# Kernel optimization log

Hardware: AMD Instinct MI355X
Metric: run time of the kernel (lower is better)

Reference implementation:

```python
import jax, jax.numpy as jnp
import numpy as np

B, S, H = 2, 2048, 2048
NH, HD = 16, 128


def _rope_tables(seq_len, dim, base=10000.0):
    inv_freq = 1.0 / (base ** (np.arange(0, dim, 2, dtype=np.float32) / dim))
    t = np.arange(seq_len, dtype=np.float32)
    freqs = np.outer(t, inv_freq)                      # [S, dim/2]
    emb = np.concatenate([freqs, freqs], axis=-1)      # [S, dim] (HF convention)
    return jnp.asarray(np.cos(emb)), jnp.asarray(np.sin(emb))


def setup_inputs() -> dict:
    key = jax.random.key(0)
    k1, k2, k3, k4, k5 = jax.random.split(key, 5)
    hidden_states = jax.random.normal(k1, (B, S, H), dtype=jnp.float32)
    # additive causal mask, broadcast over heads: (B, 1, S, S)
    causal = jnp.tril(jnp.ones((S, S), dtype=bool))
    attention_mask = jnp.where(causal, 0.0, -1e9).astype(jnp.float32)
    attention_mask = jnp.broadcast_to(attention_mask[None, None], (B, 1, S, S))
    rope_cos, rope_sin = _rope_tables(S, HD)
    scale = 1.0 / np.sqrt(H)
    Wq = jax.random.normal(k2, (H, H), dtype=jnp.float32) * scale
    Wk = jax.random.normal(k3, (H, H), dtype=jnp.float32) * scale
    Wv = jax.random.normal(k4, (H, H), dtype=jnp.float32) * scale
    Wo = jax.random.normal(k5, (H, H), dtype=jnp.float32) * scale
    return dict(hidden_states=hidden_states, attention_mask=attention_mask,
                rope_cos=rope_cos, rope_sin=rope_sin, Wq=Wq, Wk=Wk, Wv=Wv, Wo=Wo)


def _rotate_half(x):
    half = x.shape[-1] // 2
    return jnp.concatenate([-x[..., half:], x[..., :half]], axis=-1)


def reference(hidden_states, attention_mask, rope_cos, rope_sin, Wq, Wk, Wv, Wo):
    bsz, q_len, _ = hidden_states.shape
    scaling = HD ** -0.5
    # projections (torch Linear: y = x @ W.T)
    q = (hidden_states @ Wq.T).reshape(bsz, q_len, NH, HD).transpose(0, 2, 1, 3)
    k = (hidden_states @ Wk.T).reshape(bsz, q_len, NH, HD).transpose(0, 2, 1, 3)
    v = (hidden_states @ Wv.T).reshape(bsz, q_len, NH, HD).transpose(0, 2, 1, 3)
    # RoPE (rotate_half convention)
    cos = rope_cos[None, None]  # [1,1,S,HD]
    sin = rope_sin[None, None]
    q = q * cos + _rotate_half(q) * sin
    k = k * cos + _rotate_half(k) * sin
    # attention
    scores = jnp.einsum('bhqd,bhkd->bhqk', q, k) * scaling + attention_mask
    attn = jax.nn.softmax(scores.astype(jnp.float32), axis=-1).astype(q.dtype)
    out = jnp.einsum('bhqk,bhkd->bhqd', attn, v)
    out = out.transpose(0, 2, 1, 3).reshape(bsz, q_len, NH * HD)
    return out @ Wo.T
```

## Files before the change

### kernel.cpp

```cpp
#include <hip/hip_runtime.h>
#include <hip/hip_bf16.h>

typedef __bf16 bf16;
typedef __attribute__((ext_vector_type(8))) __bf16 bf16x8;
typedef __attribute__((ext_vector_type(4))) __bf16 bf16x4;
typedef __attribute__((ext_vector_type(4))) float f32x4;

#define BB 2
#define SS 2048
#define HH 2048
#define NH 16
#define HD 128

#define GLOAD_LDS16(g, l)                                                  \
    __builtin_amdgcn_global_load_lds(                                      \
        (const __attribute__((address_space(1))) void*)(g),                \
        (__attribute__((address_space(3))) void*)(l), 16, 0, 0)

__global__ __launch_bounds__(256) void cast_all(const float* __restrict__ hs,
                                                const float* __restrict__ Wq,
                                                const float* __restrict__ Wk,
                                                const float* __restrict__ Wv,
                                                const float* __restrict__ Wo,
                                                bf16* __restrict__ Xb,
                                                bf16* __restrict__ Wqkv,
                                                bf16* __restrict__ Wob) {
    const int XE4 = (BB * SS * HH) / 4;
    const int WE4 = (HH * HH) / 4;
    int i = blockIdx.x * 256 + threadIdx.x;
    const float* src;
    bf16* dst;
    int off;
    if (i < XE4) { src = hs; dst = Xb; off = i; }
    else if (i < XE4 + WE4) { src = Wq; dst = Wqkv; off = i - XE4; }
    else if (i < XE4 + 2 * WE4) { src = Wk; dst = Wqkv + (size_t)HH * HH; off = i - XE4 - WE4; }
    else if (i < XE4 + 3 * WE4) { src = Wv; dst = Wqkv + 2 * (size_t)HH * HH; off = i - XE4 - 2 * WE4; }
    else { src = Wo; dst = Wob; off = i - XE4 - 3 * WE4; }
    f32x4 v = *reinterpret_cast<const f32x4*>(src + (size_t)off * 4);
    bf16x4 o;
    o[0] = (bf16)v[0]; o[1] = (bf16)v[1]; o[2] = (bf16)v[2]; o[3] = (bf16)v[3];
    *reinterpret_cast<bf16x4*>(dst + (size_t)off * 4) = o;
}

__global__ __launch_bounds__(512, 2) void gemm256_qkv(const bf16* __restrict__ A,
                                                      const bf16* __restrict__ B,
                                                      bf16* __restrict__ Cb,
                                                      int M, int N, int K) {
    __shared__ bf16 LA[2][256 * 64];
    __shared__ bf16 LB[2][192 * 64];
    const int tid = threadIdx.x, lane = tid & 63, wave = tid >> 6;
    const int l15 = lane & 15, lhi = lane >> 4;
    const int wr = wave >> 2, wc = wave & 3;
    const int cpx = gridDim.x >> 3;
    const int wg = (blockIdx.x & 7) * cpx + (blockIdx.x >> 3);
    const int m0 = (wg & 15) * 256, n0 = (wg >> 4) * 192;
    const int NK = K >> 6;
    const int xorR = (l15 & 7) << 4;

    auto stageA = [&](int buf, int t, int h) {
        const int k0 = t << 6;
#pragma unroll
        for (int j = 0; j < 2; ++j) {
            int Xw = (h * 128 + j * 64 + wave * 8) << 7;
            int X = Xw + lane * 16;
            int T = X ^ (((X >> 7) & 7) << 4);
            GLOAD_LDS16(&A[(size_t)(m0 + (T >> 7)) * K + k0 + ((T & 127) >> 1)],
                        (char*)LA[buf] + Xw);
        }
    };
    auto stageB = [&](int buf, int t, int s) {
        const int k0 = t << 6;
        int row_base = (wave >> 1) * 48 + s * 16 + (wave & 1) * 8;
        int Xw = row_base << 7;
        int X = Xw + lane * 16;
        int T = X ^ (((X >> 7) & 7) << 4);
        GLOAD_LDS16(&B[(size_t)(n0 + (T >> 7)) * K + k0 + ((T & 127) >> 1)],
                    (char*)LB[buf] + Xw);
    };

    f32x4 acc[8][3] = {};

    stageA(0, 0, 0); stageA(0, 0, 1);
    stageB(0, 0, 0); stageB(0, 0, 1); stageB(0, 0, 2);
    stageA(1, 1, 0); stageA(1, 1, 1);
    stageB(1, 1, 0); stageB(1, 1, 1);
    asm volatile("s_waitcnt vmcnt(6)" ::: "memory");
    __builtin_amdgcn_s_barrier();

    bf16x8 af[8][2], bv[2];

#pragma unroll 1
    for (int t = 0; t < NK; ++t) {
        const int buf = t & 1;
        char* lA = (char*)LA[buf];
        char* lB = (char*)LB[buf];

#pragma unroll
        for (int mf = 0; mf < 8; ++mf)
#pragma unroll
            for (int ks = 0; ks < 2; ++ks) {
                int T = ((wr * 128 + mf * 16 + l15) << 7) + ks * 64 + lhi * 16;
                af[mf][ks] = *reinterpret_cast<const bf16x8*>(lA + (T ^ xorR));
            }
#pragma unroll
        for (int ks = 0; ks < 2; ++ks) {
            int T = ((wc * 48 + l15) << 7) + ks * 64 + lhi * 16;
            bv[ks] = *reinterpret_cast<const bf16x8*>(lB + (T ^ xorR));
        }
        if (t + 1 < NK) stageB(buf ^ 1, t + 1, 2);
        __builtin_amdgcn_s_barrier();
        __builtin_amdgcn_s_setprio(1);
#pragma unroll
        for (int mf = 0; mf < 8; ++mf)
#pragma unroll
            for (int ks = 0; ks < 2; ++ks)
                acc[mf][0] = __builtin_amdgcn_mfma_f32_16x16x32_bf16(af[mf][ks], bv[ks], acc[mf][0], 0, 0, 0);
        __builtin_amdgcn_s_setprio(0);
        __builtin_amdgcn_s_barrier();

#pragma unroll
        for (int ks = 0; ks < 2; ++ks) {
            int T = ((wc * 48 + 16 + l15) << 7) + ks * 64 + lhi * 16;
            bv[ks] = *reinterpret_cast<const bf16x8*>(lB + (T ^ xorR));
        }
        if (t + 2 < NK) { stageB(buf, t + 2, 0); stageA(buf, t + 2, 0); }
        __builtin_amdgcn_s_barrier();
        __builtin_amdgcn_s_setprio(1);
#pragma unroll
        for (int mf = 0; mf < 8; ++mf)
#pragma unroll
            for (int ks = 0; ks < 2; ++ks)
                acc[mf][1] = __builtin_amdgcn_mfma_f32_16x16x32_bf16(af[mf][ks], bv[ks], acc[mf][1], 0, 0, 0);
        __builtin_amdgcn_s_setprio(0);
        __builtin_amdgcn_s_barrier();

#pragma unroll
        for (int ks = 0; ks < 2; ++ks) {
            int T = ((wc * 48 + 32 + l15) << 7) + ks * 64 + lhi * 16;
            bv[ks] = *reinterpret_cast<const bf16x8*>(lB + (T ^ xorR));
        }
        if (t + 2 < NK) { stageB(buf, t + 2, 1); stageA(buf, t + 2, 1); }
        __builtin_amdgcn_s_barrier();
        __builtin_amdgcn_s_setprio(1);
#pragma unroll
        for (int mf = 0; mf < 8; ++mf)
#pragma unroll
            for (int ks = 0; ks < 2; ++ks)
                acc[mf][2] = __builtin_amdgcn_mfma_f32_16x16x32_bf16(af[mf][ks], bv[ks], acc[mf][2], 0, 0, 0);
        __builtin_amdgcn_s_setprio(0);
        if (t + 2 < NK) {
            asm volatile("s_waitcnt vmcnt(6)" ::: "memory");
        } else if (t + 2 == NK) {
            asm volatile("s_waitcnt vmcnt(0)" ::: "memory");
        }
        __builtin_amdgcn_s_barrier();
    }

#pragma unroll
    for (int mf = 0; mf < 8; ++mf)
#pragma unroll
        for (int nsl = 0; nsl < 3; ++nsl)
#pragma unroll
            for (int r = 0; r < 4; ++r) {
                int gm = m0 + wr * 128 + mf * 16 + lhi * 4 + r;
                int gn = n0 + wc * 48 + nsl * 16 + l15;
                int proj = gn >> 11, n2 = gn & 2047;
                int b = gm >> 11, s = gm & (SS - 1);
                int h = n2 >> 7, d = n2 & (HD - 1);
                Cb[((size_t)proj << 23) + ((((size_t)(b * NH + h)) * SS + s) << 7) + d] =
                    (bf16)acc[mf][nsl][r];
            }
}

__global__ __launch_bounds__(512, 2) void gemm_op(const bf16* __restrict__ A,
                                                  const bf16* __restrict__ B,
                                                  float* __restrict__ Cf,
                                                  int M, int N, int K) {
    __shared__ bf16 LA[2][256 * 64];
    __shared__ bf16 LB[2][128 * 64];
    const int tid = threadIdx.x, lane = tid & 63, wave = tid >> 6;
    const int l15 = lane & 15, lhi = lane >> 4;
    const int wr = wave >> 2, wc = wave & 3;
    const int cpx = gridDim.x >> 3;
    const int wg = (blockIdx.x & 7) * cpx + (blockIdx.x >> 3);
    const int m0 = (wg & 15) * 256, n0 = (wg >> 4) * 128;
    const int NK = K >> 6;
    const int xorR = (l15 & 7) << 4;

    auto stageA = [&](int buf, int t, int h) {
        const int k0 = t << 6;
#pragma unroll
        for (int j = 0; j < 2; ++j) {
            int Xw = (h * 128 + j * 64 + wave * 8) << 7;
            int X = Xw + lane * 16;
            int T = X ^ (((X >> 7) & 7) << 4);
            GLOAD_LDS16(&A[(size_t)(m0 + (T >> 7)) * K + k0 + ((T & 127) >> 1)],
                        (char*)LA[buf] + Xw);
        }
    };
    auto stageB = [&](int buf, int t, int s) {
        const int k0 = t << 6;
        int row_base = (wave >> 1) * 32 + s * 16 + (wave & 1) * 8;
        int Xw = row_base << 7;
        int X = Xw + lane * 16;
        int T = X ^ (((X >> 7) & 7) << 4);
        GLOAD_LDS16(&B[(size_t)(n0 + (T >> 7)) * K + k0 + ((T & 127) >> 1)],
                    (char*)LB[buf] + Xw);
    };

    f32x4 acc[8][2] = {};

    stageA(0, 0, 0); stageA(0, 0, 1); stageB(0, 0, 0); stageB(0, 0, 1);
    stageA(1, 1, 0); stageA(1, 1, 1); stageB(1, 1, 0);
    asm volatile("s_waitcnt vmcnt(5)" ::: "memory");
    __builtin_amdgcn_s_barrier();

    bf16x8 af[8][2], bv[2];

#pragma unroll 1
    for (int t = 0; t < NK; ++t) {
        const int buf = t & 1;
        char* lA = (char*)LA[buf];
        char* lB = (char*)LB[buf];

#pragma unroll
        for (int mf = 0; mf < 8; ++mf)
#pragma unroll
            for (int ks = 0; ks < 2; ++ks) {
                int T = ((wr * 128 + mf * 16 + l15) << 7) + ks * 64 + lhi * 16;
                af[mf][ks] = *reinterpret_cast<const bf16x8*>(lA + (T ^ xorR));
            }
#pragma unroll
        for (int ks = 0; ks < 2; ++ks) {
            int T = ((wc * 32 + l15) << 7) + ks * 64 + lhi * 16;
            bv[ks] = *reinterpret_cast<const bf16x8*>(lB + (T ^ xorR));
        }
        if (t + 1 < NK) stageB(buf ^ 1, t + 1, 1);
        __builtin_amdgcn_s_barrier();
        __builtin_amdgcn_s_setprio(1);
#pragma unroll
        for (int mf = 0; mf < 8; ++mf)
#pragma unroll
            for (int ks = 0; ks < 2; ++ks)
                acc[mf][0] = __builtin_amdgcn_mfma_f32_16x16x32_bf16(af[mf][ks], bv[ks], acc[mf][0], 0, 0, 0);
        __builtin_amdgcn_s_setprio(0);
        __builtin_amdgcn_s_barrier();

#pragma unroll
        for (int ks = 0; ks < 2; ++ks) {
            int T = ((wc * 32 + 16 + l15) << 7) + ks * 64 + lhi * 16;
            bv[ks] = *reinterpret_cast<const bf16x8*>(lB + (T ^ xorR));
        }
        if (t + 2 < NK) { stageB(buf, t + 2, 0); stageA(buf, t + 2, 0); stageA(buf, t + 2, 1); }
        __builtin_amdgcn_s_barrier();
        __builtin_amdgcn_s_setprio(1);
#pragma unroll
        for (int mf = 0; mf < 8; ++mf)
#pragma unroll
            for (int ks = 0; ks < 2; ++ks)
                acc[mf][1] = __builtin_amdgcn_mfma_f32_16x16x32_bf16(af[mf][ks], bv[ks], acc[mf][1], 0, 0, 0);
        __builtin_amdgcn_s_setprio(0);
        if (t + 2 < NK) {
            asm volatile("s_waitcnt vmcnt(5)" ::: "memory");
        } else {
            asm volatile("s_waitcnt vmcnt(0)" ::: "memory");
        }
        __builtin_amdgcn_s_barrier();
    }

#pragma unroll
    for (int mf = 0; mf < 8; ++mf)
#pragma unroll
        for (int nsl = 0; nsl < 2; ++nsl)
#pragma unroll
            for (int r = 0; r < 4; ++r) {
                int gm = m0 + wr * 128 + mf * 16 + lhi * 4 + r;
                int gn = n0 + wc * 32 + nsl * 16 + l15;
                Cf[(size_t)gm * N + gn] = acc[mf][nsl][r];
            }
}

__global__ __launch_bounds__(256) void rope_tv(bf16* __restrict__ Qh,
                                               bf16* __restrict__ Kh,
                                               const float* __restrict__ cosT,
                                               const float* __restrict__ sinT,
                                               const bf16* __restrict__ Vh,
                                               bf16* __restrict__ Vt) {
    __shared__ bf16 T[64 * 64];
    const int tid = threadIdx.x;
    if (blockIdx.x < 2048) {
        int idx = blockIdx.x * 256 + tid;
        int g = idx & 7;
        int s = (idx >> 3) & (SS - 1);
        int head = idx >> 14;
        int d0 = g * 8;
        size_t base = ((size_t)head * SS + s) * HD;
        f32x4 ca = *reinterpret_cast<const f32x4*>(&cosT[s * HD + d0]);
        f32x4 cb = *reinterpret_cast<const f32x4*>(&cosT[s * HD + d0 + 4]);
        f32x4 sa = *reinterpret_cast<const f32x4*>(&sinT[s * HD + d0]);
        f32x4 sb = *reinterpret_cast<const f32x4*>(&sinT[s * HD + d0 + 4]);
        bf16x8 ql = *reinterpret_cast<const bf16x8*>(&Qh[base + d0]);
        bf16x8 qh = *reinterpret_cast<const bf16x8*>(&Qh[base + 64 + d0]);
        bf16x8 kl = *reinterpret_cast<const bf16x8*>(&Kh[base + d0]);
        bf16x8 kh = *reinterpret_cast<const bf16x8*>(&Kh[base + 64 + d0]);
        bf16x8 qlo, qhi, klo, khi;
#pragma unroll
        for (int j = 0; j < 8; ++j) {
            float c = (j < 4) ? ca[j] : cb[j - 4];
            float sn = (j < 4) ? sa[j] : sb[j - 4];
            float q0 = (float)ql[j], q1 = (float)qh[j];
            float k0 = (float)kl[j], k1 = (float)kh[j];
            qlo[j] = (bf16)(q0 * c - q1 * sn);
            qhi[j] = (bf16)(q1 * c + q0 * sn);
            klo[j] = (bf16)(k0 * c - k1 * sn);
            khi[j] = (bf16)(k1 * c + k0 * sn);
        }
        *reinterpret_cast<bf16x8*>(&Qh[base + d0]) = qlo;
        *reinterpret_cast<bf16x8*>(&Qh[base + 64 + d0]) = qhi;
        *reinterpret_cast<bf16x8*>(&Kh[base + d0]) = klo;
        *reinterpret_cast<bf16x8*>(&Kh[base + 64 + d0]) = khi;
    } else {
        const int b2 = blockIdx.x - 2048;
        const int s0 = (b2 & 31) * 64;
        const int d0 = ((b2 >> 5) & 1) * 64;
        const int head = b2 >> 6;
        const bf16* src = Vh + ((size_t)head * SS) * HD;
        bf16* dst = Vt + ((size_t)head * HD) * SS;

#pragma unroll
        for (int i = 0; i < 2; ++i) {
            int id = tid + i * 256;
            int r = id >> 3, c16 = id & 7;
            bf16x8 v = *reinterpret_cast<const bf16x8*>(&src[(size_t)(s0 + r) * HD + d0 + c16 * 8]);
            int sw = c16 ^ ((r ^ (r >> 3)) & 7);
            *reinterpret_cast<bf16x8*>((char*)T + r * 128 + sw * 16) = v;
        }
        __syncthreads();
#pragma unroll
        for (int i = 0; i < 2; ++i) {
            int id = tid + i * 256;
            int dr = id >> 3, sc8 = (id & 7) * 8;
            bf16x8 o;
#pragma unroll
            for (int j = 0; j < 8; ++j) {
                int r = sc8 + j;
                int sw = (dr >> 3) ^ ((r ^ (r >> 3)) & 7);
                o[j] = *reinterpret_cast<const bf16*>((char*)T + r * 128 + sw * 16 + (dr & 7) * 2);
            }
            *reinterpret_cast<bf16x8*>(&dst[(size_t)(d0 + dr) * SS + s0 + sc8]) = o;
        }
    }
}

__global__ __launch_bounds__(256) void attn_kernel(const bf16* __restrict__ Q,
                                                   const bf16* __restrict__ K,
                                                   const bf16* __restrict__ Vt,
                                                   bf16* __restrict__ Ob) {
    __shared__ bf16 Ks[2][64 * 128];
    __shared__ bf16 Vs[2][128 * 64];
    __shared__ bf16 Ps[4][32 * 72];

    const int tid = threadIdx.x, lane = tid & 63, wave = tid >> 6;
    const int l15 = lane & 15, lhi = lane >> 4;
    const int bid = blockIdx.x;
    const int orig = (bid & 7) * 32 + (bid >> 3);
    const int head = orig >> 3;
    const int pi = orig & 7;
    const int b = head >> 4, h = head & (NH - 1);
    const size_t hb = (size_t)head * SS * HD;
    const bf16* Vth = Vt + (size_t)head * HD * SS;
    const float cexp = 0.08838834764831845f * 1.4426950408889634f;
    const float THR = 62.0f;

    auto stageKV = [&](int buf, int kv0) {
#pragma unroll
        for (int j = 0; j < 4; ++j) {
            int Xw = (j * 4 + wave) << 10;
            int X = Xw + lane * 16;
            int T = X ^ (((X >> 8) & 7) << 4);
            GLOAD_LDS16(&K[hb + (size_t)(kv0 + (T >> 8)) * HD + ((T & 255) >> 1)],
                        (char*)Ks[buf] + Xw);
        }
#pragma unroll
        for (int j = 0; j < 4; ++j) {
            int Xw = (j * 4 + wave) << 10;
            int X = Xw + lane * 16;
            int T = X ^ (((X >> 7) & 7) << 4);
            GLOAD_LDS16(&Vth[(size_t)(T >> 7) * SS + kv0 + ((T & 127) >> 1)],
                        (char*)Vs[buf] + Xw);
        }
    };

#pragma unroll 1
    for (int part = 0; part < 2; ++part) {
        const int t = part ? (15 - pi) : pi;
        const int q0 = t * 128;
        const int qw0 = q0 + wave * 32;
        const int nkv = 2 * t + 2;

        bf16x8 qf[2][4];
#pragma unroll
        for (int mf = 0; mf < 2; ++mf)
#pragma unroll
            for (int ks = 0; ks < 4; ++ks)
                qf[mf][ks] = *reinterpret_cast<const bf16x8*>(
                    &Q[hb + (size_t)(qw0 + mf * 16 + l15) * HD + ks * 32 + 8 * lhi]);

        f32x4 oacc[2][8] = {};
        float Mr[2][4], Lp[2][4];
#pragma unroll
        for (int mf = 0; mf < 2; ++mf)
#pragma unroll
            for (int r = 0; r < 4; ++r) { Mr[mf][r] = -INFINITY; Lp[mf][r] = 0.f; }

        stageKV(0, 0);
        asm volatile("s_waitcnt vmcnt(0)" ::: "memory");
        __builtin_amdgcn_s_barrier();

        for (int it = 0; it < nkv; ++it) {
            const int cur = it & 1;
            if (it + 1 < nkv) stageKV(cur ^ 1, (it + 1) * 64);

            f32x4 sf[2][4] = {};
#pragma unroll
            for (int ks = 0; ks < 4; ++ks) {
#pragma unroll
                for (int ne = 0; ne < 4; ++ne) {
                    int row = ne * 16 + l15;
                    bf16x8 kf = *reinterpret_cast<const bf16x8*>(
                        (const char*)Ks[cur] + ((row * 256 + (ks * 4 + lhi) * 16) ^ ((row & 7) << 4)));
#pragma unroll
                    for (int mf = 0; mf < 2; ++mf)
                        sf[mf][ne] = __builtin_amdgcn_mfma_f32_16x16x32_bf16(qf[mf][ks], kf, sf[mf][ne], 0, 0, 0);
                }
            }

            if (it >= nkv - 2) {
#pragma unroll
                for (int mf = 0; mf < 2; ++mf)
#pragma unroll
                    for (int ne = 0; ne < 4; ++ne)
#pragma unroll
                        for (int r = 0; r < 4; ++r) {
                            int gq = qw0 + mf * 16 + lhi * 4 + r;
                            int gk = it * 64 + ne * 16 + l15;
                            if (gk > gq) sf[mf][ne][r] = -INFINITY;
                        }
            }

            float lm[2][4];
            bool need = false;
#pragma unroll
            for (int mf = 0; mf < 2; ++mf)
#pragma unroll
                for (int r = 0; r < 4; ++r) {
                    lm[mf][r] = fmaxf(fmaxf(sf[mf][0][r], sf[mf][1][r]),
                                      fmaxf(sf[mf][2][r], sf[mf][3][r]));
                    need = need || (lm[mf][r] > Mr[mf][r] + THR);
                }
            if (__any(need)) {
                float rmax[2][4];
#pragma unroll
                for (int mf = 0; mf < 2; ++mf)
#pragma unroll
                    for (int r = 0; r < 4; ++r) rmax[mf][r] = lm[mf][r];
#pragma unroll
                for (int m = 1; m < 16; m <<= 1)
#pragma unroll
                    for (int mf = 0; mf < 2; ++mf)
#pragma unroll
                        for (int r = 0; r < 4; ++r)
                            rmax[mf][r] = fmaxf(rmax[mf][r], __shfl_xor(rmax[mf][r], m));
#pragma unroll
                for (int mf = 0; mf < 2; ++mf)
#pragma unroll
                    for (int r = 0; r < 4; ++r) {
                        float nM = fmaxf(Mr[mf][r], rmax[mf][r]);
                        float scf = __builtin_amdgcn_exp2f((Mr[mf][r] - nM) * cexp);
                        Mr[mf][r] = nM;
                        Lp[mf][r] *= scf;
#pragma unroll
                        for (int nf = 0; nf < 8; ++nf) oacc[mf][nf][r] *= scf;
                    }
            }
#pragma unroll
            for (int mf = 0; mf < 2; ++mf)
#pragma unroll
                for (int ne = 0; ne < 4; ++ne)
#pragma unroll
                    for (int r = 0; r < 4; ++r) {
                        float p = __builtin_amdgcn_exp2f((sf[mf][ne][r] - Mr[mf][r]) * cexp);
                        Lp[mf][r] += p;
                        Ps[wave][(mf * 16 + lhi * 4 + r) * 72 + ne * 16 + l15] = (bf16)p;
                    }

#pragma unroll
            for (int ks = 0; ks < 2; ++ks) {
                bf16x8 pa0 = *reinterpret_cast<const bf16x8*>(
                    &Ps[wave][(l15) * 72 + ks * 32 + 8 * lhi]);
                bf16x8 pa1 = *reinterpret_cast<const bf16x8*>(
                    &Ps[wave][(16 + l15) * 72 + ks * 32 + 8 * lhi]);
#pragma unroll
                for (int nf = 0; nf < 8; ++nf) {
                    int row = nf * 16 + l15;
                    bf16x8 vb = *reinterpret_cast<const bf16x8*>(
                        (const char*)Vs[cur] + ((row * 128 + (ks * 4 + lhi) * 16) ^ ((row & 7) << 4)));
                    oacc[0][nf] = __builtin_amdgcn_mfma_f32_16x16x32_bf16(pa0, vb, oacc[0][nf], 0, 0, 0);
                    oacc[1][nf] = __builtin_amdgcn_mfma_f32_16x16x32_bf16(pa1, vb, oacc[1][nf], 0, 0, 0);
                }
            }

            asm volatile("s_waitcnt vmcnt(0)" ::: "memory");
            __builtin_amdgcn_s_barrier();
        }

#pragma unroll
        for (int m = 1; m < 16; m <<= 1)
#pragma unroll
            for (int mf = 0; mf < 2; ++mf)
#pragma unroll
                for (int r = 0; r < 4; ++r)
                    Lp[mf][r] += __shfl_xor(Lp[mf][r], m);
#pragma unroll
        for (int mf = 0; mf < 2; ++mf) {
            float inv[4];
#pragma unroll
            for (int r = 0; r < 4; ++r) inv[r] = 1.f / Lp[mf][r];
#pragma unroll
            for (int nf = 0; nf < 8; ++nf)
#pragma unroll
                for (int r = 0; r < 4; ++r) {
                    int s = qw0 + mf * 16 + lhi * 4 + r;
                    int d = nf * 16 + l15;
                    Ob[((size_t)(b * SS + s)) * HH + h * HD + d] = (bf16)(oacc[mf][nf][r] * inv[r]);
                }
        }
    }
}

extern "C" void kernel_launch(void* const* d_in, const int* in_sizes, int n_in,
                              void* d_out, int out_size, void* d_ws, size_t ws_size,
                              hipStream_t stream) {
    const float* hs   = (const float*)d_in[0];
    const float* cosT = (const float*)d_in[2];
    const float* sinT = (const float*)d_in[3];
    const float* Wq   = (const float*)d_in[4];
    const float* Wk   = (const float*)d_in[5];
    const float* Wv   = (const float*)d_in[6];
    const float* Wo   = (const float*)d_in[7];
    float* out = (float*)d_out;

    char* w = (char*)d_ws;
    auto alloc = [&](size_t bytes) {
        char* p = w;
        w += (bytes + 255) & ~(size_t)255;
        return p;
    };
    const size_t XE = (size_t)BB * SS * HH;
    const size_t WE = (size_t)HH * HH;
    bf16* Xb   = (bf16*)alloc(XE * 2);
    bf16* Wqkv = (bf16*)alloc(3 * WE * 2);
    bf16* Wob  = (bf16*)alloc(WE * 2);
    bf16* QKV  = (bf16*)alloc(3 * XE * 2);
    bf16* Vtg  = (bf16*)alloc(XE * 2);
    bf16* Ob   = (bf16*)alloc(XE * 2);

    const int M = BB * SS;
    bf16* Qh = QKV;
    bf16* Kh = QKV + XE;
    bf16* Vh = QKV + 2 * XE;

    {
        int total4 = (int)((XE + 4 * WE) / 4);
        cast_all<<<(total4 + 255) / 256, 256, 0, stream>>>(hs, Wq, Wk, Wv, Wo, Xb, Wqkv, Wob);
    }

    gemm256_qkv<<<512, 512, 0, stream>>>(Xb, Wqkv, QKV, M, 3 * HH, HH);

    rope_tv<<<4096, 256, 0, stream>>>(Qh, Kh, cosT, sinT, Vh, Vtg);

    attn_kernel<<<256, 256, 0, stream>>>(Qh, Kh, Vtg, Ob);

    gemm_op<<<256, 512, 0, stream>>>(Ob, Wob, out, M, HH, HH);
}
```

Baseline: 274.0 us.

## Split attention work across 8 waves with 16 query rows each

Raises the attention block from 4 to 8 waves. Each wave now owns 16 query rows instead of 32, and the K/V staging is spread over 8 waves. This should cut per-wave register pressure and give more waves for latency hiding, since the grid has only 256 blocks. In exchange, K/V fragments read from LDS are reused across half as many MFMAs per wave, so LDS read traffic per FLOP doubles, and barrier cost grows with more waves.

```diff
diff --git a/kernel.cpp b/kernel.cpp
--- a/kernel.cpp
+++ b/kernel.cpp
@@ -352,13 +352,13 @@
     }
 }
 
-__global__ __launch_bounds__(256) void attn_kernel(const bf16* __restrict__ Q,
+__global__ __launch_bounds__(512) void attn_kernel(const bf16* __restrict__ Q,
                                                    const bf16* __restrict__ K,
                                                    const bf16* __restrict__ Vt,
                                                    bf16* __restrict__ Ob) {
     __shared__ bf16 Ks[2][64 * 128];
     __shared__ bf16 Vs[2][128 * 64];
-    __shared__ bf16 Ps[4][32 * 72];
+    __shared__ bf16 Ps[8][16 * 72];
 
     const int tid = threadIdx.x, lane = tid & 63, wave = tid >> 6;
     const int l15 = lane & 15, lhi = lane >> 4;
@@ -374,16 +374,16 @@
 
     auto stageKV = [&](int buf, int kv0) {
 #pragma unroll
-        for (int j = 0; j < 4; ++j) {
-            int Xw = (j * 4 + wave) << 10;
+        for (int j = 0; j < 2; ++j) {
+            int Xw = (j * 8 + wave) << 10;
             int X = Xw + lane * 16;
             int T = X ^ (((X >> 8) & 7) << 4);
             GLOAD_LDS16(&K[hb + (size_t)(kv0 + (T >> 8)) * HD + ((T & 255) >> 1)],
                         (char*)Ks[buf] + Xw);
         }
 #pragma unroll
-        for (int j = 0; j < 4; ++j) {
-            int Xw = (j * 4 + wave) << 10;
+        for (int j = 0; j < 2; ++j) {
+            int Xw = (j * 8 + wave) << 10;
             int X = Xw + lane * 16;
             int T = X ^ (((X >> 7) & 7) << 4);
             GLOAD_LDS16(&Vth[(size_t)(T >> 7) * SS + kv0 + ((T & 127) >> 1)],
@@ -395,23 +395,19 @@
     for (int part = 0; part < 2; ++part) {
         const int t = part ? (15 - pi) : pi;
         const int q0 = t * 128;
-        const int qw0 = q0 + wave * 32;
+        const int qw = q0 + wave * 16;
         const int nkv = 2 * t + 2;
 
-        bf16x8 qf[2][4];
-#pragma unroll
-        for (int mf = 0; mf < 2; ++mf)
-#pragma unroll
-            for (int ks = 0; ks < 4; ++ks)
-                qf[mf][ks] = *reinterpret_cast<const bf16x8*>(
-                    &Q[hb + (size_t)(qw0 + mf * 16 + l15) * HD + ks * 32 + 8 * lhi]);
-
-        f32x4 oacc[2][8] = {};
-        float Mr[2][4], Lp[2][4];
-#pragma unroll
-        for (int mf = 0; mf < 2; ++mf)
-#pragma unroll
-            for (int r = 0; r < 4; ++r) { Mr[mf][r] = -INFINITY; Lp[mf][r] = 0.f; }
+        bf16x8 qf[4];
+#pragma unroll
+        for (int ks = 0; ks < 4; ++ks)
+            qf[ks] = *reinterpret_cast<const bf16x8*>(
+                &Q[hb + (size_t)(qw + l15) * HD + ks * 32 + 8 * lhi]);
+
+        f32x4 oacc[8] = {};
+        float Mr[4], Lp[4];
+#pragma unroll
+        for (int r = 0; r < 4; ++r) { Mr[r] = -INFINITY; Lp[r] = 0.f; }
 
         stageKV(0, 0);
         asm volatile("s_waitcnt vmcnt(0)" ::: "memory");
@@ -421,7 +417,7 @@
             const int cur = it & 1;
             if (it + 1 < nkv) stageKV(cur ^ 1, (it + 1) * 64);
 
-            f32x4 sf[2][4] = {};
+            f32x4 sf[4] = {};
 #pragma unroll
             for (int ks = 0; ks < 4; ++ks) {
 #pragma unroll
@@ -429,84 +425,63 @@
                     int row = ne * 16 + l15;
                     bf16x8 kf = *reinterpret_cast<const bf16x8*>(
                         (const char*)Ks[cur] + ((row * 256 + (ks * 4 + lhi) * 16) ^ ((row & 7) << 4)));
-#pragma unroll
-                    for (int mf = 0; mf < 2; ++mf)
-                        sf[mf][ne] = __builtin_amdgcn_mfma_f32_16x16x32_bf16(qf[mf][ks], kf, sf[mf][ne], 0, 0, 0);
+                    sf[ne] = __builtin_amdgcn_mfma_f32_16x16x32_bf16(qf[ks], kf, sf[ne], 0, 0, 0);
                 }
             }
 
             if (it >= nkv - 2) {
 #pragma unroll
-                for (int mf = 0; mf < 2; ++mf)
-#pragma unroll
-                    for (int ne = 0; ne < 4; ++ne)
-#pragma unroll
-                        for (int r = 0; r < 4; ++r) {
-                            int gq = qw0 + mf * 16 + lhi * 4 + r;
-                            int gk = it * 64 + ne * 16 + l15;
-                            if (gk > gq) sf[mf][ne][r] = -INFINITY;
-                        }
-            }
-
-            float lm[2][4];
-            bool need = false;
-#pragma unroll
-            for (int mf = 0; mf < 2; ++mf)
+                for (int ne = 0; ne < 4; ++ne)
+#pragma unroll
+                    for (int r = 0; r < 4; ++r) {
+                        int gq = qw + lhi * 4 + r;
+                        int gk = it * 64 + ne * 16 + l15;
+                        if (gk > gq) sf[ne][r] = -INFINITY;
+                    }
+            }
+
+            float lm[4];
+#pragma unroll
+            for (int r = 0; r < 4; ++r)
+                lm[r] = fmaxf(fmaxf(sf[0][r], sf[1][r]), fmaxf(sf[2][r], sf[3][r]));
+            bool need = (lm[0] > Mr[0] + THR) || (lm[1] > Mr[1] + THR) ||
+                        (lm[2] > Mr[2] + THR) || (lm[3] > Mr[3] + THR);
+            if (__any(need)) {
+                float rmax[4] = {lm[0], lm[1], lm[2], lm[3]};
+#pragma unroll
+                for (int m = 1; m < 16; m <<= 1)
+#pragma unroll
+                    for (int r = 0; r < 4; ++r)
+                        rmax[r] = fmaxf(rmax[r], __shfl_xor(rmax[r], m));
 #pragma unroll
                 for (int r = 0; r < 4; ++r) {
-                    lm[mf][r] = fmaxf(fmaxf(sf[mf][0][r], sf[mf][1][r]),
-                                      fmaxf(sf[mf][2][r], sf[mf][3][r]));
-                    need = need || (lm[mf][r] > Mr[mf][r] + THR);
+                    float nM = fmaxf(Mr[r], rmax[r]);
+                    float scf = __builtin_amdgcn_exp2f((Mr[r] - nM) * cexp);
+                    Mr[r] = nM;
+                    Lp[r] *= scf;
+#pragma unroll
+                    for (int nf = 0; nf < 8; ++nf) oacc[nf][r] *= scf;
                 }
-            if (__any(need)) {
-                float rmax[2][4];
-#pragma unroll
-                for (int mf = 0; mf < 2; ++mf)
-#pragma unroll
-                    for (int r = 0; r < 4; ++r) rmax[mf][r] = lm[mf][r];
-#pragma unroll
-                for (int m = 1; m < 16; m <<= 1)
-#pragma unroll
-                    for (int mf = 0; mf < 2; ++mf)
-#pragma unroll
-                        for (int r = 0; r < 4; ++r)
-                            rmax[mf][r] = fmaxf(rmax[mf][r], __shfl_xor(rmax[mf][r], m));
-#pragma unroll
-                for (int mf = 0; mf < 2; ++mf)
-#pragma unroll
-                    for (int r = 0; r < 4; ++r) {
-                        float nM = fmaxf(Mr[mf][r], rmax[mf][r]);
-                        float scf = __builtin_amdgcn_exp2f((Mr[mf][r] - nM) * cexp);
-                        Mr[mf][r] = nM;
-                        Lp[mf][r] *= scf;
-#pragma unroll
-                        for (int nf = 0; nf < 8; ++nf) oacc[mf][nf][r] *= scf;
-                    }
-            }
-#pragma unroll
-            for (int mf = 0; mf < 2; ++mf)
-#pragma unroll
-                for (int ne = 0; ne < 4; ++ne)
-#pragma unroll
-                    for (int r = 0; r < 4; ++r) {
-                        float p = __builtin_amdgcn_exp2f((sf[mf][ne][r] - Mr[mf][r]) * cexp);
-                        Lp[mf][r] += p;
-                        Ps[wave][(mf * 16 + lhi * 4 + r) * 72 + ne * 16 + l15] = (bf16)p;
-                    }
+            }
+#pragma unroll
+            for (int ne = 0; ne < 4; ++ne)
+#pragma unroll
+                for (int r = 0; r < 4; ++r) {
+                    float p = __builtin_amdgcn_exp2f((sf[ne][r] - Mr[r]) * cexp);
+                    Lp[r] += p;
+                    Ps[wave][(lhi * 4 + r) * 72 + ne * 16 + l15] = (bf16)p;
+                }
 
 #pragma unroll
             for (int ks = 0; ks < 2; ++ks) {
-                bf16x8 pa0 = *reinterpret_cast<const bf16x8*>(
-                    &Ps[wave][(l15) * 72 + ks * 32 + 8 * lhi]);
-                bf16x8 pa1 = *reinterpret_cast<const bf16x8*>(
-                    &Ps[wave][(16 + l15) * 72 + ks * 32 + 8 * lhi]);
+                bf16x8 pa = *reinterpret_cast<const bf16x8*>(
+                    &Ps[wave][l15 * 72 + ks * 32 + 8 * lhi]);
 #pragma unroll
                 for (int nf = 0; nf < 8; ++nf) {
                     int row = nf * 16 + l15;
                     bf16x8 vb = *reinterpret_cast<const bf16x8*>(
                         (const char*)Vs[cur] + ((row * 128 + (ks * 4 + lhi) * 16) ^ ((row & 7) << 4)));
-                    oacc[0][nf] = __builtin_amdgcn_mfma_f32_16x16x32_bf16(pa0, vb, oacc[0][nf], 0, 0, 0);
-                    oacc[1][nf] = __builtin_amdgcn_mfma_f32_16x16x32_bf16(pa1, vb, oacc[1][nf], 0, 0, 0);
+                    oacc[nf] = __builtin_amdgcn_mfma_f32_16x16x32_bf16(pa, vb, oacc[nf], 0, 0, 0);
                 }
             }
 
@@ -517,24 +492,19 @@
 #pragma unroll
         for (int m = 1; m < 16; m <<= 1)
 #pragma unroll
-            for (int mf = 0; mf < 2; ++mf)
-#pragma unroll
-                for (int r = 0; r < 4; ++r)
-                    Lp[mf][r] += __shfl_xor(Lp[mf][r], m);
-#pragma unroll
-        for (int mf = 0; mf < 2; ++mf) {
-            float inv[4];
-#pragma unroll
-            for (int r = 0; r < 4; ++r) inv[r] = 1.f / Lp[mf][r];
-#pragma unroll
-            for (int nf = 0; nf < 8; ++nf)
-#pragma unroll
-                for (int r = 0; r < 4; ++r) {
-                    int s = qw0 + mf * 16 + lhi * 4 + r;
-                    int d = nf * 16 + l15;
-                    Ob[((size_t)(b * SS + s)) * HH + h * HD + d] = (bf16)(oacc[mf][nf][r] * inv[r]);
-                }
-        }
+            for (int r = 0; r < 4; ++r)
+                Lp[r] += __shfl_xor(Lp[r], m);
+        float inv[4];
+#pragma unroll
+        for (int r = 0; r < 4; ++r) inv[r] = 1.f / Lp[r];
+#pragma unroll
+        for (int nf = 0; nf < 8; ++nf)
+#pragma unroll
+            for (int r = 0; r < 4; ++r) {
+                int s = qw + lhi * 4 + r;
+                int d = nf * 16 + l15;
+                Ob[((size_t)(b * SS + s)) * HH + h * HD + d] = (bf16)(oacc[nf][r] * inv[r]);
+            }
     }
 }
 
@@ -579,7 +549,7 @@
 
     rope_tv<<<4096, 256, 0, stream>>>(Qh, Kh, cosT, sinT, Vh, Vtg);
 
-    attn_kernel<<<256, 256, 0, stream>>>(Qh, Kh, Vtg, Ob);
+    attn_kernel<<<256, 512, 0, stream>>>(Qh, Kh, Vtg, Ob);
 
     gemm_op<<<256, 512, 0, stream>>>(Ob, Wob, out, M, HH, HH);
 }
```

Measured after the change: 257.3 us, median of 2. 1.06x faster.
